# Kernel tuning notes

Measured on AMD Instinct MI355X. Metric: run time of the kernel, lower is better.

Reference implementation:

```python
import jax, jax.numpy as jnp
import numpy as np

B, S, D, H = 4, 2048, 1024, 16
HD = D // H  # head_dim = 64

def setup_inputs() -> dict:
    key = jax.random.key(0)
    ks = jax.random.split(key, 6)
    scale = 1.0 / np.sqrt(D)
    x = jax.random.normal(ks[0], (B, S, D), dtype=jnp.float32)
    Wq = jax.random.normal(ks[1], (D, D), dtype=jnp.float32) * scale
    Wk = jax.random.normal(ks[2], (D, D), dtype=jnp.float32) * scale
    Wv = jax.random.normal(ks[3], (D, D), dtype=jnp.float32) * scale
    Wo = jax.random.normal(ks[4], (D, D), dtype=jnp.float32) * scale
    z = jnp.zeros((D,), dtype=jnp.float32)
    return {"x": x, "Wq": Wq, "bq": z, "Wk": Wk, "bk": z, "Wv": Wv, "bv": z, "Wo": Wo, "bo": z}

def reference(x, Wq, bq, Wk, bk, Wv, bv, Wo, bo):
    b, s, d = x.shape
    hd = d // H
    def split_heads(t):
        return t.reshape(b, s, H, hd).swapaxes(1, 2)  # [B,H,S,hd]
    q = split_heads(x @ Wq + bq)
    k = split_heads(x @ Wk + bk)
    v = split_heads(x @ Wv + bv)
    logits = jnp.einsum('bhqd,bhkd->bhqk', q, k) / jnp.sqrt(jnp.asarray(hd, x.dtype))
    attn = jax.nn.softmax(logits, axis=-1)
    vals = jnp.einsum('bhqk,bhkd->bhqd', attn, v)
    vals = vals.swapaxes(1, 2).reshape(b, s, d)
    return vals @ Wo + bo
```

## Files before the change

kernel.cpp:

```cpp
#include <hip/hip_runtime.h>
#include <hip/hip_bf16.h>
#include <cstdint>
#include <cstddef>


typedef __attribute__((ext_vector_type(8))) short short8;
typedef __attribute__((ext_vector_type(8))) unsigned short ushort8;
typedef __attribute__((ext_vector_type(4))) unsigned short ushort4v;
typedef __attribute__((ext_vector_type(4))) float floatx4;

#define LOG2E 1.44269504088896340736f
#define QSCALE (0.125f * LOG2E)

__device__ __forceinline__ unsigned short f2bf(float f) {
  union { float f; unsigned int u; } c; c.f = f;
  return (unsigned short)((c.u + 0x7fffu + ((c.u >> 16) & 1u)) >> 16);
}

__device__ __forceinline__ unsigned int pack_bf16(float a, float b) {
  unsigned int ua = __builtin_bit_cast(unsigned int, a) + 0x8000u;
  unsigned int ub = __builtin_bit_cast(unsigned int, b) + 0x8000u;
  return __builtin_amdgcn_perm(ub, ua, 0x07060302);
}

__device__ __forceinline__ float fexp2(float x) {
#if __HIP_DEVICE_COMPILE__
  return __builtin_amdgcn_exp2f(x);
#else
  return x;
#endif
}

__device__ __forceinline__ void gl_lds16(const void* g, void* l) {
  __builtin_amdgcn_global_load_lds((__attribute__((address_space(1))) void*)g,
                                   (__attribute__((address_space(3))) void*)l, 16, 0, 0);
}

__global__ __launch_bounds__(256) void prep_kernel(
    const float* __restrict__ x, unsigned short* __restrict__ xb,
    const float* __restrict__ Wq, const float* __restrict__ Wk,
    const float* __restrict__ Wv, const float* __restrict__ Wo,
    unsigned short* __restrict__ Wqkv_t, unsigned short* __restrict__ Wo_t) {
  __shared__ float tile[32][33];
  const int bid = blockIdx.x;
  if (bid < 8192) {
    const int i = bid * 256 + threadIdx.x;
    float4 v = ((const float4*)x)[i];
    ushort4v o;
    o.x = f2bf(v.x); o.y = f2bf(v.y); o.z = f2bf(v.z); o.w = f2bf(v.w);
    ((ushort4v*)xb)[i] = o;
    return;
  }
  const int t = bid - 8192;
  const int which = t >> 10;
  const int rest = t & 1023;
  const float* src = (which == 0) ? Wq : (which == 1) ? Wk : (which == 2) ? Wv : Wo;
  unsigned short* dst = (which == 3) ? Wo_t : (Wqkv_t + (size_t)which * 1024 * 1024);
  const int bn = (rest & 31) * 32;
  const int bk = (rest >> 5) * 32;
  const int tx = threadIdx.x & 31, ty = threadIdx.x >> 5;
#pragma unroll
  for (int r = 0; r < 32; r += 8)
    tile[ty + r][tx] = src[(size_t)(bk + ty + r) * 1024 + bn + tx];
  __syncthreads();
#pragma unroll
  for (int r = 0; r < 32; r += 8)
    dst[(size_t)(bn + ty + r) * 1024 + bk + tx] = f2bf(tile[tx][ty + r]);
}

template <int MODE>
__global__ __launch_bounds__(256, 3) void gemm_bt(
    const unsigned short* __restrict__ A, const unsigned short* __restrict__ Bt,
    int M, int N, int K,
    const float* __restrict__ bias0, const float* __restrict__ bias1,
    const float* __restrict__ bias2,
    unsigned short* __restrict__ outQ, unsigned short* __restrict__ outK,
    unsigned short* __restrict__ outVt, float* __restrict__ outF) {
  __shared__ unsigned short As[128 * 32];
  __shared__ unsigned short Bs[128 * 32];

  const int tid = threadIdx.x;
  const int lane = tid & 63;
  const int wid = tid >> 6;
  const int wm = wid >> 1, wn = wid & 1;
  const int l15 = lane & 15, q4 = lane >> 4;
  const int bm = blockIdx.x * 128, bn = blockIdx.y * 128;

  const int rowL = lane >> 2;
  const int segL = (lane & 3) * 16;

  const char* Ab = (const char*)A;
  const char* Bb = (const char*)Bt;
  const size_t strideA = (size_t)K * 2;

  floatx4 acc[4][4] = {};

  for (int k0 = 0; k0 < K; k0 += 32) {
    __syncthreads();
#pragma unroll
    for (int c0 = 0; c0 < 2; ++c0) {
      const int c = wid * 2 + c0;
      gl_lds16(Ab + (size_t)(bm + c * 16 + rowL) * strideA + (size_t)k0 * 2 + segL,
               &As[c * 512]);
      gl_lds16(Bb + (size_t)(bn + c * 16 + rowL) * strideA + (size_t)k0 * 2 + segL,
               &Bs[c * 512]);
    }
    __syncthreads();

    short8 af[4], bfr[4];
#pragma unroll
    for (int i = 0; i < 4; ++i)
      af[i] = *(const short8*)&As[(wm * 64 + i * 16 + l15) * 32 + q4 * 8];
#pragma unroll
    for (int j = 0; j < 4; ++j)
      bfr[j] = *(const short8*)&Bs[(wn * 64 + j * 16 + l15) * 32 + q4 * 8];
#pragma unroll
    for (int i = 0; i < 4; ++i)
#pragma unroll
      for (int j = 0; j < 4; ++j)
        acc[i][j] = __builtin_amdgcn_mfma_f32_16x16x32_bf16(af[i], bfr[j], acc[i][j], 0, 0, 0);
  }

  if (MODE == 0) {
    __syncthreads();
    unsigned short* scr = ((wid < 2) ? As : Bs) + (wid & 1) * 2048;
    const int region = bn >> 10;
    const float* bias = (region == 0) ? bias0 : (region == 1) ? bias1 : bias2;
    const int row0b = bm + wm * 64;
    const int b = row0b >> 11;
    const int colbase = (bn + wn * 64) & 1023;
    const int h = colbase >> 6;
    const size_t bh = (size_t)(b * 16 + h);
#pragma unroll
    for (int i = 0; i < 4; ++i) {
      const int s0 = (row0b + i * 16) & 2047;
#pragma unroll
      for (int j = 0; j < 4; ++j) {
        const int col = j * 16 + l15;
        const float bb = bias[colbase + col];
#pragma unroll
        for (int r = 0; r < 4; ++r) {
          float v = acc[i][j][r] + bb;
          if (region == 0) v *= QSCALE;
          scr[(q4 * 4 + r) * 66 + col] = f2bf(v);
        }
      }
      if (region <= 1) {
        unsigned short* dst = (region == 0) ? outQ : outK;
        ushort8 v0 = *(ushort8*)&scr[l15 * 66 + q4 * 16];
        ushort8 v1 = *(ushort8*)&scr[l15 * 66 + q4 * 16 + 8];
        unsigned short* orow = dst + (bh * 2048 + s0 + l15) * 64 + q4 * 16;
        *(ushort8*)orow = v0;
        *(ushort8*)(orow + 8) = v1;
      } else {
        const int hd = lane;
        unsigned short tmp[16];
#pragma unroll
        for (int r = 0; r < 16; ++r) tmp[r] = scr[r * 66 + hd];
        ushort8 v0, v1;
#pragma unroll
        for (int r = 0; r < 8; ++r) { v0[r] = tmp[r]; v1[r] = tmp[8 + r]; }
        unsigned short* orow = outVt + (bh * 64 + hd) * 2048 + s0;
        *(ushort8*)orow = v0;
        *(ushort8*)(orow + 8) = v1;
      }
      __syncthreads();
    }
  } else {
#pragma unroll
    for (int i = 0; i < 4; ++i) {
      const int row0 = bm + wm * 64 + i * 16 + q4 * 4;
#pragma unroll
      for (int j = 0; j < 4; ++j) {
        const int gn = bn + wn * 64 + j * 16 + l15;
        const float bb = bias0[gn];
#pragma unroll
        for (int r = 0; r < 4; ++r)
          outF[(size_t)(row0 + r) * N + gn] = acc[i][j][r] + bb;
      }
    }
  }
}

__global__ __launch_bounds__(256, 4) void flash_attn(
    const unsigned short* __restrict__ Q, const unsigned short* __restrict__ Kg,
    const unsigned short* __restrict__ Vt, unsigned short* __restrict__ Oout) {
  __shared__ __align__(128) unsigned short Ks[2][64 * 64];
  __shared__ __align__(128) unsigned short Vs[2][64 * 64];

  const int tid = threadIdx.x, lane = tid & 63, wid = tid >> 6;
  const int l15 = lane & 15, q4 = lane >> 4;

  const int lid = blockIdx.x;
  const int slot = lid >> 3;
  const int bh = (lid & 7) * 8 + (slot >> 4);
  const int q0 = (slot & 15) * 128;
  const int bb = bh >> 4, hh = bh & 15;
  const size_t base = (size_t)bh * 2048 * 64;

  short8 qf[2][2];
#pragma unroll
  for (int s = 0; s < 2; ++s) {
    const unsigned short* qrow = Q + base + (size_t)(q0 + s * 64 + wid * 16 + l15) * 64;
    qf[s][0] = *(const short8*)(qrow + q4 * 8);
    qf[s][1] = *(const short8*)(qrow + 32 + q4 * 8);
  }

  union { unsigned int u[4]; short8 v; } ov;
  ov.u[0] = 0x3F803F80u; ov.u[1] = 0x3F803F80u; ov.u[2] = 0x3F803F80u; ov.u[3] = 0x3F803F80u;
  const short8 onesf = ov.v;
  const floatx4 z4 = {0.f, 0.f, 0.f, 0.f};

  const int r0 = wid * 16 + (lane >> 3);
  const int sg2 = ((lane & 7) ^ ((lane >> 3) & 7)) * 8;
  auto gpf = [](int r) {
    const int loc = r & 31;
    return (r & 32) + ((loc >> 2) & 3) * 8 + ((loc >> 4) & 1) * 4 + (loc & 3);
  };
  const unsigned short* kc0 = Kg + base + (size_t)gpf(r0) * 64 + sg2;
  const unsigned short* kc1 = Kg + base + (size_t)gpf(r0 + 8) * 64 + sg2;
  const unsigned short* vc0 = Vt + base + (size_t)r0 * 2048 + sg2;
  const unsigned short* vc1 = vc0 + 8 * 2048;

  const int wofs = wid * 1024;
  auto stage = [&](int b) {
    gl_lds16(kc0, &Ks[b][wofs]);        gl_lds16(kc1, &Ks[b][wofs + 512]);
    gl_lds16(vc0, &Vs[b][wofs]);        gl_lds16(vc1, &Vs[b][wofs + 512]);
    kc0 += 4096; kc1 += 4096; vc0 += 64; vc1 += 64;
  };

  stage(0);

  floatx4 oacc[2][4] = {};
  floatx4 lacc[2] = {};
  const int fo0 = (q4 ^ (l15 & 7)) << 3;

  const int thr = l15 * 64;
  const unsigned short* kA = &Ks[0][thr + fo0];
  const unsigned short* kB = &Ks[0][thr + (fo0 ^ 32)];
  const unsigned short* vA = &Vs[0][thr + fo0];
  const unsigned short* vB = &Vs[0][thr + (fo0 ^ 32)];

  auto body = [&](int BUF) {
    short8 pf[2][2];
#pragma unroll
    for (int c = 0; c < 2; ++c) {
      floatx4 sc[2][2];
#pragma unroll
      for (int tt = 0; tt < 2; ++tt) {
        const int t = 2 * c + tt;
        short8 kf0 = *(const short8*)(kA + BUF + t * 1024);
        short8 kf1 = *(const short8*)(kB + BUF + t * 1024);
        __builtin_amdgcn_s_setprio(1);
#pragma unroll
        for (int s = 0; s < 2; ++s) {
          floatx4 p0 = __builtin_amdgcn_mfma_f32_16x16x32_bf16(kf0, qf[s][0], z4, 0, 0, 0);
          sc[s][tt] = __builtin_amdgcn_mfma_f32_16x16x32_bf16(kf1, qf[s][1], p0, 0, 0, 0);
        }
        __builtin_amdgcn_s_setprio(0);
      }
#pragma unroll
      for (int s = 0; s < 2; ++s) {
        float e0 = fexp2(sc[s][0][0]), e1 = fexp2(sc[s][0][1]);
        float e2 = fexp2(sc[s][0][2]), e3 = fexp2(sc[s][0][3]);
        float e4 = fexp2(sc[s][1][0]), e5 = fexp2(sc[s][1][1]);
        float e6 = fexp2(sc[s][1][2]), e7 = fexp2(sc[s][1][3]);
        union { unsigned int u[4]; short8 v; } cv;
        cv.u[0] = pack_bf16(e0, e1); cv.u[1] = pack_bf16(e2, e3);
        cv.u[2] = pack_bf16(e4, e5); cv.u[3] = pack_bf16(e6, e7);
        pf[s][c] = cv.v;
        lacc[s] = __builtin_amdgcn_mfma_f32_16x16x32_bf16(onesf, pf[s][c], lacc[s], 0, 0, 0);
      }
    }

#pragma unroll
    for (int t = 0; t < 4; ++t) {
      short8 vf0 = *(const short8*)(vA + BUF + t * 1024);
      short8 vf1 = *(const short8*)(vB + BUF + t * 1024);
      __builtin_amdgcn_s_setprio(1);
#pragma unroll
      for (int s = 0; s < 2; ++s) {
        oacc[s][t] = __builtin_amdgcn_mfma_f32_16x16x32_bf16(vf0, pf[s][0], oacc[s][t], 0, 0, 0);
        oacc[s][t] = __builtin_amdgcn_mfma_f32_16x16x32_bf16(vf1, pf[s][1], oacc[s][t], 0, 0, 0);
      }
      __builtin_amdgcn_s_setprio(0);
    }
  };

  for (int ip = 0; ip < 16; ++ip) {
    __syncthreads();
    stage(1);
    body(0);
    __syncthreads();
    if (ip < 15) stage(0);
    body(4096);
  }

#pragma unroll
  for (int s = 0; s < 2; ++s) {
    const float inv = 1.0f / lacc[s][0];
    const int srow = q0 + s * 64 + wid * 16 + l15;
    unsigned short* orow = Oout + ((size_t)bb * 2048 + srow) * 1024 + hh * 64;
#pragma unroll
    for (int t = 0; t < 4; ++t) {
      union { unsigned int u[2]; ushort4v s4; } cv;
      cv.u[0] = pack_bf16(oacc[s][t][0] * inv, oacc[s][t][1] * inv);
      cv.u[1] = pack_bf16(oacc[s][t][2] * inv, oacc[s][t][3] * inv);
      *(ushort4v*)(orow + t * 16 + q4 * 4) = cv.s4;
    }
  }
}

extern "C" void kernel_launch(void* const* d_in, const int* in_sizes, int n_in,
                              void* d_out, int out_size, void* d_ws, size_t ws_size,
                              hipStream_t stream) {
  const float* x  = (const float*)d_in[0];
  const float* Wq = (const float*)d_in[1];
  const float* bq = (const float*)d_in[2];
  const float* Wk = (const float*)d_in[3];
  const float* bk = (const float*)d_in[4];
  const float* Wv = (const float*)d_in[5];
  const float* bv = (const float*)d_in[6];
  const float* Wo = (const float*)d_in[7];
  const float* bo = (const float*)d_in[8];
  float* out = (float*)d_out;

  char* ws = (char*)d_ws;
  unsigned short* xb     = (unsigned short*)(ws);
  unsigned short* wqkv_t = (unsigned short*)(ws + (16u << 20));
  unsigned short* wo_t   = (unsigned short*)(ws + (22u << 20));
  unsigned short* Qb     = (unsigned short*)(ws + (24u << 20));
  unsigned short* Kb     = (unsigned short*)(ws + (40u << 20));
  unsigned short* Vtb    = (unsigned short*)(ws + (56u << 20));
  unsigned short* attn   = (unsigned short*)(ws + (72u << 20));
  (void)in_sizes; (void)n_in; (void)out_size; (void)ws_size;

  prep_kernel<<<dim3(12288), 256, 0, stream>>>(x, xb, Wq, Wk, Wv, Wo, wqkv_t, wo_t);
  gemm_bt<0><<<dim3(64, 24), 256, 0, stream>>>(xb, wqkv_t, 8192, 3072, 1024,
                                               bq, bk, bv, Qb, Kb, Vtb, nullptr);
  flash_attn<<<dim3(1024), 256, 0, stream>>>(Qb, Kb, Vtb, attn);
  gemm_bt<1><<<dim3(64, 8), 256, 0, stream>>>(attn, wo_t, 8192, 1024, 1024,
                                              bo, nullptr, nullptr,
                                              nullptr, nullptr, nullptr, out);
}
```

Measured before the change: 281.1 us.

## Replace QKV projection GEMM with 256x256-tile, 8-wave double-buffered kernel

The QKV projection moves to a dedicated kernel with 256x256 output tiles, 512 threads and a K-step of 64. It uses XOR-swizzled LDS layouts and a two-stage global-to-LDS double buffer with explicit waitcnt and barrier scheduling. MFMA bursts are wrapped in setprio. The goal is more data reuse per tile, more MFMA work per LDS load, and hiding global load latency. In exchange it uses 128KB of LDS per block and launches only 384 blocks, so occupancy and tail effects could suffer. The output GEMM is split out unchanged as its own kernel.

```diff
diff --git a/kernel.cpp b/kernel.cpp
--- a/kernel.cpp
+++ b/kernel.cpp
@@ -68,14 +68,149 @@
     dst[(size_t)(bn + ty + r) * 1024 + bk + tx] = f2bf(tile[tx][ty + r]);
 }
 
-template <int MODE>
-__global__ __launch_bounds__(256, 3) void gemm_bt(
+__global__ __launch_bounds__(512, 2) void gemm_qkv8(
     const unsigned short* __restrict__ A, const unsigned short* __restrict__ Bt,
-    int M, int N, int K,
-    const float* __restrict__ bias0, const float* __restrict__ bias1,
-    const float* __restrict__ bias2,
+    const float* __restrict__ bq, const float* __restrict__ bk, const float* __restrict__ bv,
     unsigned short* __restrict__ outQ, unsigned short* __restrict__ outK,
-    unsigned short* __restrict__ outVt, float* __restrict__ outF) {
+    unsigned short* __restrict__ outVt) {
+  __shared__ __align__(128) unsigned short S[65536];
+
+  const int tid = threadIdx.x, lane = tid & 63, wid = tid >> 6;
+  const int wm = wid >> 2, wn = wid & 3;
+  const int l15 = lane & 15, q4 = lane >> 4;
+  const int bm = blockIdx.x * 256, bn = blockIdx.y * 256;
+
+  const int srow = wid * 16 + (lane >> 3);
+  const int sgu = ((lane & 7) ^ ((lane >> 3) & 7)) * 8;
+  const unsigned short* pa00 = A + (size_t)(bm + srow) * 1024 + sgu;
+  const unsigned short* pa01 = pa00 + 8 * 1024;
+  const unsigned short* pa10 = pa00 + 128 * 1024;
+  const unsigned short* pa11 = pa00 + 136 * 1024;
+  const unsigned short* pb00 = Bt + (size_t)(bn + srow) * 1024 + sgu;
+  const unsigned short* pb01 = pb00 + 8 * 1024;
+  const unsigned short* pb10 = pb00 + 128 * 1024;
+  const unsigned short* pb11 = pb00 + 136 * 1024;
+
+  const int wdst = wid * 1024;
+  auto stage = [&](const int SO) {
+    gl_lds16(pa00, &S[SO + wdst]);          gl_lds16(pa01, &S[SO + wdst + 512]);
+    gl_lds16(pa10, &S[SO + 8192 + wdst]);   gl_lds16(pa11, &S[SO + 8192 + wdst + 512]);
+    gl_lds16(pb00, &S[32768 + SO + wdst]);        gl_lds16(pb01, &S[32768 + SO + wdst + 512]);
+    gl_lds16(pb10, &S[32768 + SO + 8192 + wdst]); gl_lds16(pb11, &S[32768 + SO + 8192 + wdst + 512]);
+    pa00 += 64; pa01 += 64; pa10 += 64; pa11 += 64;
+    pb00 += 64; pb01 += 64; pb10 += 64; pb11 += 64;
+  };
+
+  const int fo0 = (q4 ^ (l15 & 7)) * 8;
+  const unsigned short* aP0 = S + wm * 8192 + l15 * 64 + fo0;
+  const unsigned short* aP1 = S + wm * 8192 + l15 * 64 + (fo0 ^ 32);
+  const unsigned short* bP0 = S + 32768 + (wn >> 1) * 8192 + ((wn & 1) * 64 + l15) * 64 + fo0;
+  const unsigned short* bP1 = S + 32768 + (wn >> 1) * 8192 + ((wn & 1) * 64 + l15) * 64 + (fo0 ^ 32);
+
+  floatx4 acc[8][4] = {};
+
+  stage(0); stage(16384);
+  asm volatile("s_waitcnt vmcnt(8)" ::: "memory");
+  __builtin_amdgcn_sched_barrier(0);
+  __builtin_amdgcn_s_barrier();
+  __builtin_amdgcn_sched_barrier(0);
+
+  auto compute = [&](const int RO) {
+#pragma unroll
+    for (int kk = 0; kk < 2; ++kk) {
+      const unsigned short* aP = kk ? aP1 : aP0;
+      const unsigned short* bP = kk ? bP1 : bP0;
+      short8 af[8], bf[4];
+#pragma unroll
+      for (int i = 0; i < 8; ++i) af[i] = *(const short8*)(aP + RO + i * 1024);
+#pragma unroll
+      for (int j = 0; j < 4; ++j) bf[j] = *(const short8*)(bP + RO + j * 1024);
+      asm volatile("s_waitcnt lgkmcnt(0)" ::: "memory");
+      __builtin_amdgcn_sched_barrier(0);
+      __builtin_amdgcn_s_setprio(1);
+#pragma unroll
+      for (int i = 0; i < 8; ++i)
+#pragma unroll
+        for (int j = 0; j < 4; ++j)
+          acc[i][j] = __builtin_amdgcn_mfma_f32_16x16x32_bf16(af[i], bf[j], acc[i][j], 0, 0, 0);
+      __builtin_amdgcn_s_setprio(0);
+    }
+  };
+
+#define QKV_BDRY(SO)                                         \
+  __builtin_amdgcn_sched_barrier(0);                         \
+  __builtin_amdgcn_s_barrier();                              \
+  __builtin_amdgcn_sched_barrier(0);                         \
+  stage(SO);                                                 \
+  asm volatile("s_waitcnt vmcnt(8)" ::: "memory");           \
+  __builtin_amdgcn_sched_barrier(0);                         \
+  __builtin_amdgcn_s_barrier();                              \
+  __builtin_amdgcn_sched_barrier(0);
+
+  for (int p = 0; p < 7; ++p) {
+    compute(0);
+    QKV_BDRY(0)
+    compute(16384);
+    QKV_BDRY(16384)
+  }
+  compute(0);
+  __builtin_amdgcn_sched_barrier(0);
+  __builtin_amdgcn_s_barrier();
+  asm volatile("s_waitcnt vmcnt(0)" ::: "memory");
+  __builtin_amdgcn_sched_barrier(0);
+  __builtin_amdgcn_s_barrier();
+  __builtin_amdgcn_sched_barrier(0);
+  compute(16384);
+#undef QKV_BDRY
+
+  __syncthreads();
+  unsigned short* scr = S + wid * 1088;
+  const int region = bn >> 10;
+  const float* bias = (region == 0) ? bq : (region == 1) ? bk : bv;
+  const int row0b = bm + wm * 128;
+  const int b = row0b >> 11;
+  const int colbase = (bn + wn * 64) & 1023;
+  const int h = colbase >> 6;
+  const size_t bh = (size_t)(b * 16 + h);
+#pragma unroll
+  for (int i = 0; i < 8; ++i) {
+    const int s0 = (row0b + i * 16) & 2047;
+#pragma unroll
+    for (int j = 0; j < 4; ++j) {
+      const int col = j * 16 + l15;
+      const float bb = bias[colbase + col];
+#pragma unroll
+      for (int r = 0; r < 4; ++r) {
+        float v = acc[i][j][r] + bb;
+        if (region == 0) v *= QSCALE;
+        scr[(q4 * 4 + r) * 66 + col] = f2bf(v);
+      }
+    }
+    if (region <= 1) {
+      unsigned short* dst = (region == 0) ? outQ : outK;
+      ushort8 v0 = *(ushort8*)&scr[l15 * 66 + q4 * 16];
+      ushort8 v1 = *(ushort8*)&scr[l15 * 66 + q4 * 16 + 8];
+      unsigned short* orow = dst + (bh * 2048 + s0 + l15) * 64 + q4 * 16;
+      *(ushort8*)orow = v0;
+      *(ushort8*)(orow + 8) = v1;
+    } else {
+      const int hd = lane;
+      unsigned short tmp[16];
+#pragma unroll
+      for (int r = 0; r < 16; ++r) tmp[r] = scr[r * 66 + hd];
+      ushort8 v0, v1;
+#pragma unroll
+      for (int r = 0; r < 8; ++r) { v0[r] = tmp[r]; v1[r] = tmp[8 + r]; }
+      unsigned short* orow = outVt + (bh * 64 + hd) * 2048 + s0;
+      *(ushort8*)orow = v0;
+      *(ushort8*)(orow + 8) = v1;
+    }
+  }
+}
+
+__global__ __launch_bounds__(256, 3) void gemm_o(
+    const unsigned short* __restrict__ A, const unsigned short* __restrict__ Bt,
+    int M, int N, int K, const float* __restrict__ bias0, float* __restrict__ outF) {
   __shared__ unsigned short As[128 * 32];
   __shared__ unsigned short Bs[128 * 32];
 
@@ -121,63 +256,16 @@
         acc[i][j] = __builtin_amdgcn_mfma_f32_16x16x32_bf16(af[i], bfr[j], acc[i][j], 0, 0, 0);
   }
 
-  if (MODE == 0) {
-    __syncthreads();
-    unsigned short* scr = ((wid < 2) ? As : Bs) + (wid & 1) * 2048;
-    const int region = bn >> 10;
-    const float* bias = (region == 0) ? bias0 : (region == 1) ? bias1 : bias2;
-    const int row0b = bm + wm * 64;
-    const int b = row0b >> 11;
-    const int colbase = (bn + wn * 64) & 1023;
-    const int h = colbase >> 6;
-    const size_t bh = (size_t)(b * 16 + h);
-#pragma unroll
-    for (int i = 0; i < 4; ++i) {
-      const int s0 = (row0b + i * 16) & 2047;
-#pragma unroll
-      for (int j = 0; j < 4; ++j) {
-        const int col = j * 16 + l15;
-        const float bb = bias[colbase + col];
-#pragma unroll
-        for (int r = 0; r < 4; ++r) {
-          float v = acc[i][j][r] + bb;
-          if (region == 0) v *= QSCALE;
-          scr[(q4 * 4 + r) * 66 + col] = f2bf(v);
-        }
-      }
-      if (region <= 1) {
-        unsigned short* dst = (region == 0) ? outQ : outK;
-        ushort8 v0 = *(ushort8*)&scr[l15 * 66 + q4 * 16];
-        ushort8 v1 = *(ushort8*)&scr[l15 * 66 + q4 * 16 + 8];
-        unsigned short* orow = dst + (bh * 2048 + s0 + l15) * 64 + q4 * 16;
-        *(ushort8*)orow = v0;
-        *(ushort8*)(orow + 8) = v1;
-      } else {
-        const int hd = lane;
-        unsigned short tmp[16];
-#pragma unroll
-        for (int r = 0; r < 16; ++r) tmp[r] = scr[r * 66 + hd];
-        ushort8 v0, v1;
-#pragma unroll
-        for (int r = 0; r < 8; ++r) { v0[r] = tmp[r]; v1[r] = tmp[8 + r]; }
-        unsigned short* orow = outVt + (bh * 64 + hd) * 2048 + s0;
-        *(ushort8*)orow = v0;
-        *(ushort8*)(orow + 8) = v1;
-      }
-      __syncthreads();
-    }
-  } else {
-#pragma unroll
-    for (int i = 0; i < 4; ++i) {
-      const int row0 = bm + wm * 64 + i * 16 + q4 * 4;
-#pragma unroll
-      for (int j = 0; j < 4; ++j) {
-        const int gn = bn + wn * 64 + j * 16 + l15;
-        const float bb = bias0[gn];
-#pragma unroll
-        for (int r = 0; r < 4; ++r)
-          outF[(size_t)(row0 + r) * N + gn] = acc[i][j][r] + bb;
-      }
+#pragma unroll
+  for (int i = 0; i < 4; ++i) {
+    const int row0 = bm + wm * 64 + i * 16 + q4 * 4;
+#pragma unroll
+    for (int j = 0; j < 4; ++j) {
+      const int gn = bn + wn * 64 + j * 16 + l15;
+      const float bb = bias0[gn];
+#pragma unroll
+      for (int r = 0; r < 4; ++r)
+        outF[(size_t)(row0 + r) * N + gn] = acc[i][j][r] + bb;
     }
   }
 }
@@ -336,10 +424,7 @@
   (void)in_sizes; (void)n_in; (void)out_size; (void)ws_size;
 
   prep_kernel<<<dim3(12288), 256, 0, stream>>>(x, xb, Wq, Wk, Wv, Wo, wqkv_t, wo_t);
-  gemm_bt<0><<<dim3(64, 24), 256, 0, stream>>>(xb, wqkv_t, 8192, 3072, 1024,
-                                               bq, bk, bv, Qb, Kb, Vtb, nullptr);
+  gemm_qkv8<<<dim3(32, 12), 512, 0, stream>>>(xb, wqkv_t, bq, bk, bv, Qb, Kb, Vtb);
   flash_attn<<<dim3(1024), 256, 0, stream>>>(Qb, Kb, Vtb, attn);
-  gemm_bt<1><<<dim3(64, 8), 256, 0, stream>>>(attn, wo_t, 8192, 1024, 1024,
-                                              bo, nullptr, nullptr,
-                                              nullptr, nullptr, nullptr, out);
-}
+  gemm_o<<<dim3(64, 8), 256, 0, stream>>>(attn, wo_t, 8192, 1024, 1024, bo, out);
+}
```

After: 270.4 us. -3.8%, faster.

## Double-buffer GEMM K-loop with BK=64, swizzled LDS and async prefetch

Applied to the files above, without the earlier changes.

Replaces the single-buffered 128x128x32 GEMM loop with a double-buffered BK=64 pipeline. Each stage's global-to-LDS loads are issued while the other buffer is being computed, using partial vmcnt waits and raw s_barriers. LDS rows get an XOR swizzle to cut bank conflicts, and MFMA bursts are wrapped in setprio. K is hardcoded to 1024, and the larger 64KB shared buffer lowers occupancy to 2 blocks per CU.

```diff
diff --git a/kernel.cpp b/kernel.cpp
--- a/kernel.cpp
+++ b/kernel.cpp
@@ -69,61 +69,100 @@
 }
 
 template <int MODE>
-__global__ __launch_bounds__(256, 3) void gemm_bt(
-    const unsigned short* __restrict__ A, const unsigned short* __restrict__ Bt,
-    int M, int N, int K,
+__global__ __launch_bounds__(256, 2) void gemm128(
+    const unsigned short* __restrict__ A, const unsigned short* __restrict__ Bt, int N,
     const float* __restrict__ bias0, const float* __restrict__ bias1,
     const float* __restrict__ bias2,
     unsigned short* __restrict__ outQ, unsigned short* __restrict__ outK,
     unsigned short* __restrict__ outVt, float* __restrict__ outF) {
-  __shared__ unsigned short As[128 * 32];
-  __shared__ unsigned short Bs[128 * 32];
-
-  const int tid = threadIdx.x;
-  const int lane = tid & 63;
-  const int wid = tid >> 6;
+  __shared__ __align__(128) unsigned short S[32768];
+
+  const int tid = threadIdx.x, lane = tid & 63, wid = tid >> 6;
   const int wm = wid >> 1, wn = wid & 1;
   const int l15 = lane & 15, q4 = lane >> 4;
   const int bm = blockIdx.x * 128, bn = blockIdx.y * 128;
 
-  const int rowL = lane >> 2;
-  const int segL = (lane & 3) * 16;
-
-  const char* Ab = (const char*)A;
-  const char* Bb = (const char*)Bt;
-  const size_t strideA = (size_t)K * 2;
+  const int srow = wid * 32 + (lane >> 3);
+  const int sgu = ((lane & 7) ^ ((lane >> 3) & 7)) * 8;
+  const unsigned short* pa = A + (size_t)(bm + srow) * 1024 + sgu;
+  const unsigned short* pb = Bt + (size_t)(bn + srow) * 1024 + sgu;
+
+  const int wdst = wid * 2048;
+  auto stage = [&](const int SO) {
+#pragma unroll
+    for (int m = 0; m < 4; ++m)
+      gl_lds16(pa + (size_t)m * 8192, &S[SO + wdst + m * 512]);
+#pragma unroll
+    for (int m = 0; m < 4; ++m)
+      gl_lds16(pb + (size_t)m * 8192, &S[16384 + SO + wdst + m * 512]);
+    pa += 64; pb += 64;
+  };
+
+  const int fo0 = (q4 ^ (l15 & 7)) * 8;
+  const unsigned short* aP0 = S + (wm * 64 + l15) * 64 + fo0;
+  const unsigned short* aP1 = S + (wm * 64 + l15) * 64 + (fo0 ^ 32);
+  const unsigned short* bP0 = S + 16384 + (wn * 64 + l15) * 64 + fo0;
+  const unsigned short* bP1 = S + 16384 + (wn * 64 + l15) * 64 + (fo0 ^ 32);
 
   floatx4 acc[4][4] = {};
 
-  for (int k0 = 0; k0 < K; k0 += 32) {
-    __syncthreads();
-#pragma unroll
-    for (int c0 = 0; c0 < 2; ++c0) {
-      const int c = wid * 2 + c0;
-      gl_lds16(Ab + (size_t)(bm + c * 16 + rowL) * strideA + (size_t)k0 * 2 + segL,
-               &As[c * 512]);
-      gl_lds16(Bb + (size_t)(bn + c * 16 + rowL) * strideA + (size_t)k0 * 2 + segL,
-               &Bs[c * 512]);
-    }
-    __syncthreads();
-
-    short8 af[4], bfr[4];
-#pragma unroll
-    for (int i = 0; i < 4; ++i)
-      af[i] = *(const short8*)&As[(wm * 64 + i * 16 + l15) * 32 + q4 * 8];
-#pragma unroll
-    for (int j = 0; j < 4; ++j)
-      bfr[j] = *(const short8*)&Bs[(wn * 64 + j * 16 + l15) * 32 + q4 * 8];
-#pragma unroll
-    for (int i = 0; i < 4; ++i)
-#pragma unroll
-      for (int j = 0; j < 4; ++j)
-        acc[i][j] = __builtin_amdgcn_mfma_f32_16x16x32_bf16(af[i], bfr[j], acc[i][j], 0, 0, 0);
-  }
+  stage(0); stage(8192);
+  asm volatile("s_waitcnt vmcnt(8)" ::: "memory");
+  __builtin_amdgcn_sched_barrier(0);
+  __builtin_amdgcn_s_barrier();
+  __builtin_amdgcn_sched_barrier(0);
+
+  auto compute = [&](const int RO) {
+#pragma unroll
+    for (int kk = 0; kk < 2; ++kk) {
+      const unsigned short* aP = kk ? aP1 : aP0;
+      const unsigned short* bP = kk ? bP1 : bP0;
+      short8 af[4], bf[4];
+#pragma unroll
+      for (int i = 0; i < 4; ++i) af[i] = *(const short8*)(aP + RO + i * 1024);
+#pragma unroll
+      for (int j = 0; j < 4; ++j) bf[j] = *(const short8*)(bP + RO + j * 1024);
+      asm volatile("s_waitcnt lgkmcnt(0)" ::: "memory");
+      __builtin_amdgcn_sched_barrier(0);
+      __builtin_amdgcn_s_setprio(1);
+#pragma unroll
+      for (int i = 0; i < 4; ++i)
+#pragma unroll
+        for (int j = 0; j < 4; ++j)
+          acc[i][j] = __builtin_amdgcn_mfma_f32_16x16x32_bf16(af[i], bf[j], acc[i][j], 0, 0, 0);
+      __builtin_amdgcn_s_setprio(0);
+    }
+  };
+
+#define G128_BDRY(SO)                                        \
+  __builtin_amdgcn_sched_barrier(0);                         \
+  __builtin_amdgcn_s_barrier();                              \
+  __builtin_amdgcn_sched_barrier(0);                         \
+  stage(SO);                                                 \
+  asm volatile("s_waitcnt vmcnt(8)" ::: "memory");           \
+  __builtin_amdgcn_sched_barrier(0);                         \
+  __builtin_amdgcn_s_barrier();                              \
+  __builtin_amdgcn_sched_barrier(0);
+
+  for (int p = 0; p < 7; ++p) {
+    compute(0);
+    G128_BDRY(0)
+    compute(8192);
+    G128_BDRY(8192)
+  }
+  compute(0);
+  __builtin_amdgcn_sched_barrier(0);
+  __builtin_amdgcn_s_barrier();
+  asm volatile("s_waitcnt vmcnt(0)" ::: "memory");
+  __builtin_amdgcn_sched_barrier(0);
+  __builtin_amdgcn_s_barrier();
+  __builtin_amdgcn_sched_barrier(0);
+  compute(8192);
+#undef G128_BDRY
 
   if (MODE == 0) {
     __syncthreads();
-    unsigned short* scr = ((wid < 2) ? As : Bs) + (wid & 1) * 2048;
+    unsigned short* scr = S + wid * 1088;
     const int region = bn >> 10;
     const float* bias = (region == 0) ? bias0 : (region == 1) ? bias1 : bias2;
     const int row0b = bm + wm * 64;
@@ -336,10 +375,9 @@
   (void)in_sizes; (void)n_in; (void)out_size; (void)ws_size;
 
   prep_kernel<<<dim3(12288), 256, 0, stream>>>(x, xb, Wq, Wk, Wv, Wo, wqkv_t, wo_t);
-  gemm_bt<0><<<dim3(64, 24), 256, 0, stream>>>(xb, wqkv_t, 8192, 3072, 1024,
-                                               bq, bk, bv, Qb, Kb, Vtb, nullptr);
+  gemm128<0><<<dim3(64, 24), 256, 0, stream>>>(xb, wqkv_t, 3072, bq, bk, bv,
+                                               Qb, Kb, Vtb, nullptr);
   flash_attn<<<dim3(1024), 256, 0, stream>>>(Qb, Kb, Vtb, attn);
-  gemm_bt<1><<<dim3(64, 8), 256, 0, stream>>>(attn, wo_t, 8192, 1024, 1024,
-                                              bo, nullptr, nullptr,
+  gemm128<1><<<dim3(64, 8), 256, 0, stream>>>(attn, wo_t, 1024, bo, nullptr, nullptr,
                                               nullptr, nullptr, nullptr, out);
 }
```

New measurement: 260.8 us. 1.08x faster.
